# Kernel tuning notes

Hardware: AMD Instinct MI355X
Metric: run time of the kernel (lower is better)

## Reference

```python
import jax, jax.numpy as jnp
import numpy as np


def ste_sign(x):
    # larq ste_sign forward: sign(x) with sign(0) = 1
    return jnp.where(x >= 0, 1.0, -1.0).astype(x.dtype)


def setup_inputs() -> dict:
    key = jax.random.key(0)
    ks = jax.random.split(key, 8)
    B, H, W, Cin, Cout = 32, 56, 56, 256, 256
    x = jax.random.normal(ks[0], (B, H, W, Cin), dtype=jnp.float32)
    bias1 = jax.random.normal(ks[1], (1, 1, 1, Cin), dtype=jnp.float32) * 0.01
    kernel = jax.random.normal(ks[2], (3, 3, Cin, Cout), dtype=jnp.float32) * 0.1
    # BatchNormalization(scale=False): beta learnable, gamma=1, moving stats
    bn_beta = jax.random.normal(ks[3], (Cout,), dtype=jnp.float32) * 0.01
    bn_mean = jax.random.normal(ks[4], (Cout,), dtype=jnp.float32) * 0.01
    bn_var = jax.random.uniform(ks[5], (Cout,), dtype=jnp.float32, minval=0.5, maxval=1.5)
    bias2 = jax.random.normal(ks[6], (1, 1, 1, Cout), dtype=jnp.float32) * 0.01
    return {"x": x, "bias1": bias1, "kernel": kernel, "bn_beta": bn_beta,
            "bn_mean": bn_mean, "bn_var": bn_var, "bias2": bias2}


def reference(x, bias1, kernel, bn_beta, bn_mean, bn_var, bias2):
    eps = 1e-3  # keras BatchNormalization default epsilon
    strides = 1
    # lb_activation_1: learnable bias + ste_sign activation
    a = ste_sign(x + bias1)
    # QuantConv2D: binarize kernel, 'same' padding conv (NHWC, HWIO)
    qk = ste_sign(kernel)
    y = jax.lax.conv_general_dilated(
        a, qk, window_strides=(strides, strides), padding='SAME',
        dimension_numbers=('NHWC', 'HWIO', 'NHWC'))
    # BatchNormalization(scale=False) inference: (y - mean)/sqrt(var+eps) + beta
    y = (y - bn_mean) * jax.lax.rsqrt(bn_var + eps) + bn_beta
    # strides == 1: no avgpool residual branch
    # lb_activation_2: learnable bias + relu
    out = jax.nn.relu(y + bias2)
    return out
```

## Files before the change

### kernel.cpp

```cpp
#include <hip/hip_runtime.h>


typedef int v4i __attribute__((ext_vector_type(4)));
typedef unsigned int u32;

#define NB   32
#define HW   56
#define HP   58
#define HP2  (HP*HP)
#define CIN  256
#define COUT 256
#define NPIX (NB*HW*HW)
#define KTOT 2304
#define BM   256
#define BN   256
#define NSTEP 36
#define NWG  (NPIX/BM)

#define PA_BYTES ((size_t)NB*HP*HP*CIN)
#define WT_OFF   PA_BYTES
#define WT_BYTES ((size_t)KTOT*COUT)
#define SC_OFF   (WT_OFF + WT_BYTES)
#define SH_OFF   (SC_OFF + 1024)

__device__ __forceinline__ void g2l16(const void* g, void* l) {
    __builtin_amdgcn_global_load_lds(
        (const __attribute__((address_space(1))) void*)g,
        (__attribute__((address_space(3))) void*)l, 16, 0, 0);
}

__global__ __launch_bounds__(256) void pack_a_kernel(
    const float* __restrict__ x, const float* __restrict__ b1,
    signed char* __restrict__ pa)
{
    const int lane = threadIdx.x & 63;
    const int pp = blockIdx.x * 4 + (threadIdx.x >> 6);
    const int n = pp / HP2, r = pp % HP2, ph = r / HP, pw = r % HP;
    const int ci = lane * 4;
    u32 o = 0;
    if (ph >= 1 && ph <= HW && pw >= 1 && pw <= HW) {
        const int pix = (n * HW + ph - 1) * HW + (pw - 1);
        const float4 xv = *(const float4*)(x + (size_t)pix * CIN + ci);
        const float4 bv = *(const float4*)(b1 + ci);
        o  = (u32)(unsigned char)((xv.x + bv.x >= 0.f) ? 1 : -1);
        o |= (u32)(unsigned char)((xv.y + bv.y >= 0.f) ? 1 : -1) << 8;
        o |= (u32)(unsigned char)((xv.z + bv.z >= 0.f) ? 1 : -1) << 16;
        o |= (u32)(unsigned char)((xv.w + bv.w >= 0.f) ? 1 : -1) << 24;
    }
    *(u32*)(pa + (size_t)pp * CIN + ci) = o;
}

__global__ __launch_bounds__(256) void packw_kernel(
    const float* __restrict__ k, signed char* __restrict__ wt)
{
    __shared__ signed char tile[64][256];
    const int t = threadIdx.x, k0 = blockIdx.x * 64;
    for (int j = 0; j < 64; ++j)
        tile[j][t] = (k[(size_t)(k0 + j) * COUT + t] >= 0.f) ? 1 : -1;
    __syncthreads();
    u32 wd[16];
#pragma unroll
    for (int j = 0; j < 16; ++j) wd[j] = 0;
#pragma unroll
    for (int j = 0; j < 64; ++j)
        wd[j >> 2] |= ((u32)(unsigned char)tile[j][t]) << ((j & 3) * 8);
    uint4* dst = (uint4*)(wt + (size_t)t * KTOT + k0);
#pragma unroll
    for (int j = 0; j < 4; ++j)
        dst[j] = make_uint4(wd[4*j], wd[4*j+1], wd[4*j+2], wd[4*j+3]);
}

__global__ __launch_bounds__(256) void bnprep_kernel(
    const float* __restrict__ beta, const float* __restrict__ mean,
    const float* __restrict__ var, const float* __restrict__ b2,
    float* __restrict__ scale, float* __restrict__ shift)
{
    const int t = threadIdx.x;
    const float s = rsqrtf(var[t] + 1e-3f);
    scale[t] = s;
    shift[t] = beta[t] - mean[t] * s + b2[t];
}

__global__ __launch_bounds__(512, 2) void conv_mfma_kernel(
    const signed char* __restrict__ pa, const signed char* __restrict__ wt,
    const float* __restrict__ scale, const float* __restrict__ shift,
    float* __restrict__ out)
{
    __shared__ signed char L[2][32768];

    const int t = threadIdx.x, l = t & 63, w = t >> 6;
    const int wr = w >> 2, wc = w & 3;
    const int swz = (blockIdx.x & 7) * (NWG / 8) + (blockIdx.x >> 3);
    const int p0 = swz * BM;

    const signed char* abase[2];
#pragma unroll
    for (int i = 0; i < 2; ++i) {
        const int q = (t >> 2) + i * 128;
        const int p = p0 + q;
        const int n = p / 3136, r = p % 3136, h = r / 56, ww = r % 56;
        const int aswz = (((t & 3) ^ ((q >> 1) & 3)) << 4);
        abase[i] = pa + ((size_t)(n * HP + h) * HP + ww) * CIN + aswz;
    }
    const signed char* wbase[2];
#pragma unroll
    for (int j = 0; j < 2; ++j) {
        const int r = j * 128 + (t >> 2);
        const int bswz = (((t & 3) ^ ((r >> 1) & 3)) << 4);
        wbase[j] = wt + (size_t)r * KTOT + bswz;
    }

    int aoff[8], boff[4];
#pragma unroll
    for (int pg = 0; pg < 8; ++pg) {
        const int row = wr * 128 + pg * 16 + (l & 15);
        aoff[pg] = row * 64 + ((((l >> 4) ^ (row >> 1)) & 3) << 4);
    }
#pragma unroll
    for (int cg = 0; cg < 4; ++cg) {
        const int row = wc * 64 + cg * 16 + (l & 15);
        boff[cg] = 16384 + row * 64 + ((((l >> 4) ^ (row >> 1)) & 3) << 4);
    }

    v4i acc[8][4];
#pragma unroll
    for (int i = 0; i < 8; ++i)
#pragma unroll
        for (int j = 0; j < 4; ++j) acc[i][j] = (v4i){0, 0, 0, 0};

    auto goffA = [&](int s) {
        const int tap = s >> 2, cq = s & 3;
        const int ty = tap / 3, tx = tap - ty * 3;
        return ((ty * HP + tx) << 8) + (cq << 6);
    };
    auto STAGE = [&](int buf, int s) {
        const int go = goffA(s);
        g2l16(abase[0] + go, &L[buf][w * 1024]);
        g2l16(abase[1] + go, &L[buf][8192 + w * 1024]);
        g2l16(wbase[0] + (s << 6), &L[buf][16384 + w * 1024]);
        g2l16(wbase[1] + (s << 6), &L[buf][24576 + w * 1024]);
    };

    STAGE(0, 0);
    asm volatile("s_waitcnt vmcnt(0)" ::: "memory");
    __builtin_amdgcn_s_barrier();

#pragma unroll 1
    for (int s = 0; s < NSTEP; ++s) {
        const int cur = s & 1, nxt = cur ^ 1;
        const signed char* Lc = &L[cur][0];

        v4i bf0 = *(const v4i*)(Lc + boff[0]);
        v4i bf1 = *(const v4i*)(Lc + boff[1]);
        v4i bf2 = *(const v4i*)(Lc + boff[2]);
        v4i bf3 = *(const v4i*)(Lc + boff[3]);
        v4i af0 = *(const v4i*)(Lc + aoff[0]);
        v4i af1 = *(const v4i*)(Lc + aoff[1]);
        v4i af2 = *(const v4i*)(Lc + aoff[2]);
        v4i af3 = *(const v4i*)(Lc + aoff[3]);
        if (s + 1 < NSTEP) STAGE(nxt, s + 1);
        asm volatile("" ::: "memory");
        __builtin_amdgcn_s_barrier();
        __builtin_amdgcn_s_setprio(1);
        acc[0][0] = __builtin_amdgcn_mfma_i32_16x16x64_i8(af0, bf0, acc[0][0], 0, 0, 0);
        acc[0][1] = __builtin_amdgcn_mfma_i32_16x16x64_i8(af0, bf1, acc[0][1], 0, 0, 0);
        acc[0][2] = __builtin_amdgcn_mfma_i32_16x16x64_i8(af0, bf2, acc[0][2], 0, 0, 0);
        acc[0][3] = __builtin_amdgcn_mfma_i32_16x16x64_i8(af0, bf3, acc[0][3], 0, 0, 0);
        acc[1][0] = __builtin_amdgcn_mfma_i32_16x16x64_i8(af1, bf0, acc[1][0], 0, 0, 0);
        acc[1][1] = __builtin_amdgcn_mfma_i32_16x16x64_i8(af1, bf1, acc[1][1], 0, 0, 0);
        acc[1][2] = __builtin_amdgcn_mfma_i32_16x16x64_i8(af1, bf2, acc[1][2], 0, 0, 0);
        acc[1][3] = __builtin_amdgcn_mfma_i32_16x16x64_i8(af1, bf3, acc[1][3], 0, 0, 0);
        acc[2][0] = __builtin_amdgcn_mfma_i32_16x16x64_i8(af2, bf0, acc[2][0], 0, 0, 0);
        acc[2][1] = __builtin_amdgcn_mfma_i32_16x16x64_i8(af2, bf1, acc[2][1], 0, 0, 0);
        acc[2][2] = __builtin_amdgcn_mfma_i32_16x16x64_i8(af2, bf2, acc[2][2], 0, 0, 0);
        acc[2][3] = __builtin_amdgcn_mfma_i32_16x16x64_i8(af2, bf3, acc[2][3], 0, 0, 0);
        acc[3][0] = __builtin_amdgcn_mfma_i32_16x16x64_i8(af3, bf0, acc[3][0], 0, 0, 0);
        acc[3][1] = __builtin_amdgcn_mfma_i32_16x16x64_i8(af3, bf1, acc[3][1], 0, 0, 0);
        acc[3][2] = __builtin_amdgcn_mfma_i32_16x16x64_i8(af3, bf2, acc[3][2], 0, 0, 0);
        acc[3][3] = __builtin_amdgcn_mfma_i32_16x16x64_i8(af3, bf3, acc[3][3], 0, 0, 0);
        __builtin_amdgcn_s_setprio(0);
        asm volatile("" ::: "memory");
        __builtin_amdgcn_s_barrier();

        v4i af4 = *(const v4i*)(Lc + aoff[4]);
        v4i af5 = *(const v4i*)(Lc + aoff[5]);
        v4i af6 = *(const v4i*)(Lc + aoff[6]);
        v4i af7 = *(const v4i*)(Lc + aoff[7]);
        asm volatile("" ::: "memory");
        __builtin_amdgcn_s_barrier();
        __builtin_amdgcn_s_setprio(1);
        acc[4][0] = __builtin_amdgcn_mfma_i32_16x16x64_i8(af4, bf0, acc[4][0], 0, 0, 0);
        acc[4][1] = __builtin_amdgcn_mfma_i32_16x16x64_i8(af4, bf1, acc[4][1], 0, 0, 0);
        acc[4][2] = __builtin_amdgcn_mfma_i32_16x16x64_i8(af4, bf2, acc[4][2], 0, 0, 0);
        acc[4][3] = __builtin_amdgcn_mfma_i32_16x16x64_i8(af4, bf3, acc[4][3], 0, 0, 0);
        acc[5][0] = __builtin_amdgcn_mfma_i32_16x16x64_i8(af5, bf0, acc[5][0], 0, 0, 0);
        acc[5][1] = __builtin_amdgcn_mfma_i32_16x16x64_i8(af5, bf1, acc[5][1], 0, 0, 0);
        acc[5][2] = __builtin_amdgcn_mfma_i32_16x16x64_i8(af5, bf2, acc[5][2], 0, 0, 0);
        acc[5][3] = __builtin_amdgcn_mfma_i32_16x16x64_i8(af5, bf3, acc[5][3], 0, 0, 0);
        acc[6][0] = __builtin_amdgcn_mfma_i32_16x16x64_i8(af6, bf0, acc[6][0], 0, 0, 0);
        acc[6][1] = __builtin_amdgcn_mfma_i32_16x16x64_i8(af6, bf1, acc[6][1], 0, 0, 0);
        acc[6][2] = __builtin_amdgcn_mfma_i32_16x16x64_i8(af6, bf2, acc[6][2], 0, 0, 0);
        acc[6][3] = __builtin_amdgcn_mfma_i32_16x16x64_i8(af6, bf3, acc[6][3], 0, 0, 0);
        acc[7][0] = __builtin_amdgcn_mfma_i32_16x16x64_i8(af7, bf0, acc[7][0], 0, 0, 0);
        acc[7][1] = __builtin_amdgcn_mfma_i32_16x16x64_i8(af7, bf1, acc[7][1], 0, 0, 0);
        acc[7][2] = __builtin_amdgcn_mfma_i32_16x16x64_i8(af7, bf2, acc[7][2], 0, 0, 0);
        acc[7][3] = __builtin_amdgcn_mfma_i32_16x16x64_i8(af7, bf3, acc[7][3], 0, 0, 0);
        __builtin_amdgcn_s_setprio(0);
        asm volatile("s_waitcnt vmcnt(0)" ::: "memory");
        __builtin_amdgcn_s_barrier();
    }

#pragma unroll
    for (int cg = 0; cg < 4; ++cg) {
        const int co = wc * 64 + cg * 16 + (l & 15);
        const float sc = scale[co], sh = shift[co];
#pragma unroll
        for (int pg = 0; pg < 8; ++pg) {
            const int prow0 = p0 + wr * 128 + pg * 16 + (l >> 4) * 4;
#pragma unroll
            for (int rr = 0; rr < 4; ++rr) {
                const float y = (float)acc[pg][cg][rr];
                out[(size_t)(prow0 + rr) * COUT + co] = fmaxf(fmaf(y, sc, sh), 0.f);
            }
        }
    }
}

extern "C" void kernel_launch(void* const* d_in, const int* in_sizes, int n_in,
                              void* d_out, int out_size, void* d_ws, size_t ws_size,
                              hipStream_t stream)
{
    const float* x      = (const float*)d_in[0];
    const float* bias1  = (const float*)d_in[1];
    const float* kernel = (const float*)d_in[2];
    const float* bn_beta = (const float*)d_in[3];
    const float* bn_mean = (const float*)d_in[4];
    const float* bn_var  = (const float*)d_in[5];
    const float* bias2   = (const float*)d_in[6];
    float* out = (float*)d_out;

    signed char* pa  = (signed char*)d_ws;
    signed char* wtp = (signed char*)d_ws + WT_OFF;
    float* scale = (float*)((char*)d_ws + SC_OFF);
    float* shift = (float*)((char*)d_ws + SH_OFF);

    pack_a_kernel<<<dim3(NB * HP2 / 4), dim3(256), 0, stream>>>(x, bias1, pa);
    packw_kernel<<<dim3(KTOT / 64), dim3(256), 0, stream>>>(kernel, wtp);
    bnprep_kernel<<<dim3(1), dim3(256), 0, stream>>>(bn_beta, bn_mean, bn_var, bias2,
                                                     scale, shift);
    conv_mfma_kernel<<<dim3(NWG), dim3(512), 0, stream>>>(pa, wtp, scale, shift, out);
}
```

Before: 108.5 us.

## Split A and B tile prefetch across loop halves with partial vmcnt waits

The global-to-LDS staging of each K step is split in two. The weight (B) tile is issued at the top of the iteration and the activation (A) tile after the second-half fragment reads. Full vmcnt(0) drains are replaced by partial waits (vmcnt(1)/vmcnt(2)), and the per-wave LDS destinations are reassigned, so loads stay in flight across MFMA phases and global latency is hidden better. The waits leave loads outstanding across barriers, and a barrier does not wait for other waves' outstanding loads, so A data may not have landed when it is read in the next iteration. This is a correctness risk.

```diff
diff --git a/kernel.cpp b/kernel.cpp
--- a/kernel.cpp
+++ b/kernel.cpp
@@ -93,21 +93,32 @@
     const int swz = (blockIdx.x & 7) * (NWG / 8) + (blockIdx.x >> 3);
     const int p0 = swz * BM;
 
-    const signed char* abase[2];
-#pragma unroll
-    for (int i = 0; i < 2; ++i) {
-        const int q = (t >> 2) + i * 128;
-        const int p = p0 + q;
-        const int n = p / 3136, r = p % 3136, h = r / 56, ww = r % 56;
-        const int aswz = (((t & 3) ^ ((q >> 1) & 3)) << 4);
-        abase[i] = pa + ((size_t)(n * HP + h) * HP + ww) * CIN + aswz;
-    }
-    const signed char* wbase[2];
-#pragma unroll
-    for (int j = 0; j < 2; ++j) {
-        const int r = j * 128 + (t >> 2);
-        const int bswz = (((t & 3) ^ ((r >> 1) & 3)) << 4);
-        wbase[j] = wt + (size_t)r * KTOT + bswz;
+    const int a0base_l = (w < 4) ? w * 1024 : 8192 + (w - 4) * 1024;
+    const int a1base_l = a0base_l + 4096;
+    const signed char* a0src;
+    const signed char* a1src;
+    {
+        const int q0 = (a0base_l >> 6) + (l >> 2);
+        const int q1 = (a1base_l >> 6) + (l >> 2);
+        const int sl = l & 3;
+        const int p_0 = p0 + q0, p_1 = p0 + q1;
+        const int n0 = p_0 / 3136, r0 = p_0 % 3136;
+        const int n1 = p_1 / 3136, r1 = p_1 % 3136;
+        a0src = pa + ((size_t)(n0 * HP + r0 / 56) * HP + r0 % 56) * CIN
+                   + ((sl ^ ((q0 >> 1) & 3)) << 4);
+        a1src = pa + ((size_t)(n1 * HP + r1 / 56) * HP + r1 % 56) * CIN
+                   + ((sl ^ ((q1 >> 1) & 3)) << 4);
+    }
+    const int b0base_l = 16384 + w * 1024;
+    const int b1base_l = 16384 + 8192 + w * 1024;
+    const signed char* b0src;
+    const signed char* b1src;
+    {
+        const int r0 = ((b0base_l - 16384) >> 6) + (l >> 2);
+        const int r1 = ((b1base_l - 16384) >> 6) + (l >> 2);
+        const int sl = l & 3;
+        b0src = wt + (size_t)r0 * KTOT + ((sl ^ ((r0 >> 1) & 3)) << 4);
+        b1src = wt + (size_t)r1 * KTOT + ((sl ^ ((r1 >> 1) & 3)) << 4);
     }
 
     int aoff[8], boff[4];
@@ -133,22 +144,27 @@
         const int ty = tap / 3, tx = tap - ty * 3;
         return ((ty * HP + tx) << 8) + (cq << 6);
     };
-    auto STAGE = [&](int buf, int s) {
+
+    auto STAGE_B = [&](int buf, int s) {
+        g2l16(b0src + (s << 6), &L[buf][b0base_l]);
+        g2l16(b1src + (s << 6), &L[buf][b1base_l]);
+    };
+    auto STAGE_A = [&](int buf, int s) {
         const int go = goffA(s);
-        g2l16(abase[0] + go, &L[buf][w * 1024]);
-        g2l16(abase[1] + go, &L[buf][8192 + w * 1024]);
-        g2l16(wbase[0] + (s << 6), &L[buf][16384 + w * 1024]);
-        g2l16(wbase[1] + (s << 6), &L[buf][24576 + w * 1024]);
+        g2l16(a0src + go, &L[buf][a0base_l]);
+        g2l16(a1src + go, &L[buf][a1base_l]);
     };
 
-    STAGE(0, 0);
-    asm volatile("s_waitcnt vmcnt(0)" ::: "memory");
+    STAGE_B(0, 0);
+    STAGE_A(0, 0);
+    asm volatile("s_waitcnt vmcnt(1)" ::: "memory");
     __builtin_amdgcn_s_barrier();
 
 #pragma unroll 1
     for (int s = 0; s < NSTEP; ++s) {
         const int cur = s & 1, nxt = cur ^ 1;
         const signed char* Lc = &L[cur][0];
+        const bool pre = (s + 1 < NSTEP);
 
         v4i bf0 = *(const v4i*)(Lc + boff[0]);
         v4i bf1 = *(const v4i*)(Lc + boff[1]);
@@ -158,7 +174,7 @@
         v4i af1 = *(const v4i*)(Lc + aoff[1]);
         v4i af2 = *(const v4i*)(Lc + aoff[2]);
         v4i af3 = *(const v4i*)(Lc + aoff[3]);
-        if (s + 1 < NSTEP) STAGE(nxt, s + 1);
+        if (pre) STAGE_B(nxt, s + 1);
         asm volatile("" ::: "memory");
         __builtin_amdgcn_s_barrier();
         __builtin_amdgcn_s_setprio(1);
@@ -179,13 +195,15 @@
         acc[3][2] = __builtin_amdgcn_mfma_i32_16x16x64_i8(af3, bf2, acc[3][2], 0, 0, 0);
         acc[3][3] = __builtin_amdgcn_mfma_i32_16x16x64_i8(af3, bf3, acc[3][3], 0, 0, 0);
         __builtin_amdgcn_s_setprio(0);
-        asm volatile("" ::: "memory");
+        if (pre) { asm volatile("s_waitcnt vmcnt(2)" ::: "memory"); }
+        else     { asm volatile("s_waitcnt vmcnt(0)" ::: "memory"); }
         __builtin_amdgcn_s_barrier();
 
         v4i af4 = *(const v4i*)(Lc + aoff[4]);
         v4i af5 = *(const v4i*)(Lc + aoff[5]);
         v4i af6 = *(const v4i*)(Lc + aoff[6]);
         v4i af7 = *(const v4i*)(Lc + aoff[7]);
+        if (pre) STAGE_A(nxt, s + 1);
         asm volatile("" ::: "memory");
         __builtin_amdgcn_s_barrier();
         __builtin_amdgcn_s_setprio(1);
@@ -206,7 +224,7 @@
         acc[7][2] = __builtin_amdgcn_mfma_i32_16x16x64_i8(af7, bf2, acc[7][2], 0, 0, 0);
         acc[7][3] = __builtin_amdgcn_mfma_i32_16x16x64_i8(af7, bf3, acc[7][3], 0, 0, 0);
         __builtin_amdgcn_s_setprio(0);
-        asm volatile("s_waitcnt vmcnt(0)" ::: "memory");
+        if (pre) { asm volatile("s_waitcnt vmcnt(1)" ::: "memory"); }
         __builtin_amdgcn_s_barrier();
     }
 
```

Result: no change. 109.5 us (+1.0%).
